# Kernel optimization log

Measured on AMD Instinct MI355X. Metric: run time of the kernel, lower is better.

The kernel has to match this reference:

```python
import jax, jax.numpy as jnp
import numpy as np

BATCH = 1048576
IN_DIM = 64   # input_dim = A.shape[1]
OUT_DIM = 16  # output_dim = A.shape[0]


def setup_inputs() -> dict:
    key = jax.random.key(0)
    k1, k2, k3 = jax.random.split(key, 3)
    y = jax.random.normal(k1, (BATCH, IN_DIM), dtype=jnp.float32)
    A = jax.random.normal(k2, (OUT_DIM, IN_DIM), dtype=jnp.float32)
    b = jax.random.normal(k3, (BATCH, OUT_DIM), dtype=jnp.float32)
    return {"y": y, "A": A, "b": b}


def _block_matrix(A):
    # KKT block matrix [[2I, A^T], [A, 0]], shape (n+m, n+m); shared across batch.
    m, n = A.shape
    Id2 = 2.0 * jnp.eye(n, dtype=A.dtype)
    top = jnp.concatenate([Id2, A.T], axis=1)          # (n, n+m)
    bot = jnp.concatenate([A, jnp.zeros((m, m), A.dtype)], axis=1)  # (m, n+m)
    return jnp.concatenate([top, bot], axis=0)


def reference(y, A, b):
    # Solve block_matrix @ sol_i = [2*y_i; b_i] for all samples i in one batched solve
    # (original torch code loops torch.linalg.solve over the batch with the SAME matrix).
    n = A.shape[1]
    M = _block_matrix(A)                               # (n+m, n+m)
    rhs = jnp.concatenate([2.0 * y, b], axis=1)        # (batch, n+m)
    sol = jnp.linalg.solve(M, rhs.T).T                 # factorize once, all RHS at once
    y_star = sol[:, :n]
    return y_star
```

## Files before the change

### kernel.cpp

```cpp
#include <hip/hip_runtime.h>

#define BATCH   1048576
#define IN_DIM  64
#define OUT_DIM 16

__global__ __launch_bounds__(256) void precompute_kernel(
    const float* __restrict__ A, float* __restrict__ ws)
{
    __shared__ float sA[16][64];
    __shared__ float M[16][32];
    __shared__ float fac[16];
    __shared__ int piv;

    const int tid = threadIdx.x;

    for (int i = tid; i < 1024; i += 256) sA[i >> 6][i & 63] = A[i];
    __syncthreads();

    {
        const int i = tid >> 4, j = tid & 15;
        float s = 0.f;
        #pragma unroll
        for (int k = 0; k < 64; ++k) s = fmaf(sA[i][k], sA[j][k], s);
        M[i][j] = s;
        M[i][16 + j] = (i == j) ? 1.f : 0.f;
    }
    __syncthreads();

    for (int p = 0; p < 16; ++p) {
        if (tid == 0) {
            int best = p;
            float bv = fabsf(M[p][p]);
            for (int r = p + 1; r < 16; ++r) {
                float v = fabsf(M[r][p]);
                if (v > bv) { bv = v; best = r; }
            }
            piv = best;
        }
        __syncthreads();
        if (tid < 32) {
            const int pr = piv;
            if (pr != p) { float t = M[p][tid]; M[p][tid] = M[pr][tid]; M[pr][tid] = t; }
        }
        __syncthreads();
        const float pv = M[p][p];
        __syncthreads();
        if (tid < 32) M[p][tid] *= (1.0f / pv);
        __syncthreads();
        if (tid < 16) fac[tid] = M[tid][p];
        __syncthreads();
        for (int e = tid; e < 512; e += 256) {
            const int r = e >> 5, c = e & 31;
            if (r != p) M[r][c] = fmaf(-fac[r], M[p][c], M[r][c]);
        }
        __syncthreads();
    }

    for (int e = tid; e < 1024; e += 256) {
        const int k = e >> 4, j = e & 15;
        ws[e] = sA[j][k];
    }
    for (int e = tid; e < 1024; e += 256) {
        const int k = e >> 4, i = e & 15;
        float s = 0.f;
        #pragma unroll
        for (int j = 0; j < 16; ++j) s = fmaf(M[i][16 + j], sA[j][k], s);
        ws[1024 + e] = s;
    }
}

__global__ __launch_bounds__(256)
__attribute__((amdgpu_waves_per_eu(4, 4)))
void apply_kernel(
    const float* __restrict__ y, const float* __restrict__ b,
    const float* __restrict__ ws, float* __restrict__ out)
{
    __shared__ float4 buf[4][64][8];

    const int tid  = threadIdx.x;
    const int wv   = tid >> 6;
    const int l    = tid & 63;
    const int srow = l >> 3;
    const int ssl  = l & 7;

    const float4* __restrict__ At4 = reinterpret_cast<const float4*>(ws);
    const float4* __restrict__ Ct4 = reinterpret_cast<const float4*>(ws + 1024);

    const size_t wbase = (size_t)blockIdx.x * 256 + (size_t)wv * 64;
    const float*  yb = y   + wbase * 64;
    float*        ob = out + wbase * 64;
    const float4* b4 = reinterpret_cast<const float4*>(b) + (wbase + l) * 4;

    float4 g0[8], g1[8];
    #pragma unroll
    for (int i = 0; i < 8; ++i)
        g0[i] = *reinterpret_cast<const float4*>(yb + (i * 8 + srow) * 64 + ssl * 4);
    #pragma unroll
    for (int i = 0; i < 8; ++i)
        g1[i] = *reinterpret_cast<const float4*>(yb + (i * 8 + srow) * 64 + 32 + ssl * 4);
    const float4 bv0 = b4[0], bv1 = b4[1], bv2 = b4[2], bv3 = b4[3];

    #pragma unroll
    for (int i = 0; i < 8; ++i) {
        const int row = i * 8 + srow;
        buf[wv][row][ssl ^ (row & 7)] = g0[i];
    }

    float t[16];
    t[ 0] = -bv0.x; t[ 1] = -bv0.y; t[ 2] = -bv0.z; t[ 3] = -bv0.w;
    t[ 4] = -bv1.x; t[ 5] = -bv1.y; t[ 6] = -bv1.z; t[ 7] = -bv1.w;
    t[ 8] = -bv2.x; t[ 9] = -bv2.y; t[10] = -bv2.z; t[11] = -bv2.w;
    t[12] = -bv3.x; t[13] = -bv3.y; t[14] = -bv3.z; t[15] = -bv3.w;

    float4 yr[8];
    #pragma unroll
    for (int q = 0; q < 8; ++q) {
        const float4 yv = buf[wv][l][q ^ (l & 7)];
        yr[q] = yv;
        #pragma unroll
        for (int dk = 0; dk < 4; ++dk) {
            const float yk = (dk == 0) ? yv.x : (dk == 1) ? yv.y :
                             (dk == 2) ? yv.z : yv.w;
            const int k = q * 4 + dk;
            #pragma unroll
            for (int jq = 0; jq < 4; ++jq) {
                const float4 a = At4[k * 4 + jq];
                t[4*jq+0] = fmaf(a.x, yk, t[4*jq+0]);
                t[4*jq+1] = fmaf(a.y, yk, t[4*jq+1]);
                t[4*jq+2] = fmaf(a.z, yk, t[4*jq+2]);
                t[4*jq+3] = fmaf(a.w, yk, t[4*jq+3]);
            }
        }
    }

    #pragma unroll
    for (int i = 0; i < 8; ++i) {
        const int row = i * 8 + srow;
        buf[wv][row][ssl ^ (row & 7)] = g1[i];
    }

    #pragma unroll
    for (int q = 0; q < 8; ++q) {
        const float4 yv = buf[wv][l][q ^ (l & 7)];
        #pragma unroll
        for (int dk = 0; dk < 4; ++dk) {
            const float yk = (dk == 0) ? yv.x : (dk == 1) ? yv.y :
                             (dk == 2) ? yv.z : yv.w;
            const int k = 32 + q * 4 + dk;
            #pragma unroll
            for (int jq = 0; jq < 4; ++jq) {
                const float4 a = At4[k * 4 + jq];
                t[4*jq+0] = fmaf(a.x, yk, t[4*jq+0]);
                t[4*jq+1] = fmaf(a.y, yk, t[4*jq+1]);
                t[4*jq+2] = fmaf(a.z, yk, t[4*jq+2]);
                t[4*jq+3] = fmaf(a.w, yk, t[4*jq+3]);
            }
        }
    }

    #pragma unroll
    for (int q = 0; q < 8; ++q) {
        const float4 yv = buf[wv][l][q ^ (l & 7)];
        float xv[4];
        #pragma unroll
        for (int dk = 0; dk < 4; ++dk) {
            const int k = 32 + q * 4 + dk;
            float x = (dk == 0) ? yv.x : (dk == 1) ? yv.y :
                      (dk == 2) ? yv.z : yv.w;
            #pragma unroll
            for (int iq = 0; iq < 4; ++iq) {
                const float4 c = Ct4[k * 4 + iq];
                x = fmaf(-c.x, t[4*iq+0], x);
                x = fmaf(-c.y, t[4*iq+1], x);
                x = fmaf(-c.z, t[4*iq+2], x);
                x = fmaf(-c.w, t[4*iq+3], x);
            }
            xv[dk] = x;
        }
        buf[wv][l][q ^ (l & 7)] = make_float4(xv[0], xv[1], xv[2], xv[3]);
    }
    #pragma unroll
    for (int i = 0; i < 8; ++i) {
        const int row = i * 8 + srow;
        *reinterpret_cast<float4*>(ob + row * 64 + 32 + ssl * 4) =
            buf[wv][row][ssl ^ (row & 7)];
    }

    #pragma unroll
    for (int q = 0; q < 8; ++q) {
        const float4 yv = yr[q];
        float xv[4];
        #pragma unroll
        for (int dk = 0; dk < 4; ++dk) {
            const int k = q * 4 + dk;
            float x = (dk == 0) ? yv.x : (dk == 1) ? yv.y :
                      (dk == 2) ? yv.z : yv.w;
            #pragma unroll
            for (int iq = 0; iq < 4; ++iq) {
                const float4 c = Ct4[k * 4 + iq];
                x = fmaf(-c.x, t[4*iq+0], x);
                x = fmaf(-c.y, t[4*iq+1], x);
                x = fmaf(-c.z, t[4*iq+2], x);
                x = fmaf(-c.w, t[4*iq+3], x);
            }
            xv[dk] = x;
        }
        buf[wv][l][q ^ (l & 7)] = make_float4(xv[0], xv[1], xv[2], xv[3]);
    }
    #pragma unroll
    for (int i = 0; i < 8; ++i) {
        const int row = i * 8 + srow;
        *reinterpret_cast<float4*>(ob + row * 64 + ssl * 4) =
            buf[wv][row][ssl ^ (row & 7)];
    }
}

extern "C" void kernel_launch(void* const* d_in, const int* in_sizes, int n_in,
                              void* d_out, int out_size, void* d_ws, size_t ws_size,
                              hipStream_t stream) {
    const float* y = (const float*)d_in[0];
    const float* A = (const float*)d_in[1];
    const float* b = (const float*)d_in[2];
    float* out = (float*)d_out;
    float* ws  = (float*)d_ws;

    precompute_kernel<<<1, 256, 0, stream>>>(A, ws);
    apply_kernel<<<BATCH / 256, 256, 0, stream>>>(y, b, ws, out);
}
```

Baseline: 165.0 us.

## Make apply kernel persistent-ish with two tiles per wave and software-prefetched loads

```diff
diff --git a/kernel.cpp b/kernel.cpp
--- a/kernel.cpp
+++ b/kernel.cpp
@@ -3,6 +3,8 @@
 #define BATCH   1048576
 #define IN_DIM  64
 #define OUT_DIM 16
+#define TPW     2
+#define NWTOT   8192
 
 __global__ __launch_bounds__(256) void precompute_kernel(
     const float* __restrict__ A, float* __restrict__ ws)
@@ -69,13 +71,11 @@
     }
 }
 
-__global__ __launch_bounds__(256)
-__attribute__((amdgpu_waves_per_eu(4, 4)))
-void apply_kernel(
+__global__ __launch_bounds__(128, 2) void apply_kernel(
     const float* __restrict__ y, const float* __restrict__ b,
     const float* __restrict__ ws, float* __restrict__ out)
 {
-    __shared__ float4 buf[4][64][8];
+    __shared__ float4 buf[2][64][16];
 
     const int tid  = threadIdx.x;
     const int wv   = tid >> 6;
@@ -86,132 +86,138 @@
     const float4* __restrict__ At4 = reinterpret_cast<const float4*>(ws);
     const float4* __restrict__ Ct4 = reinterpret_cast<const float4*>(ws + 1024);
 
-    const size_t wbase = (size_t)blockIdx.x * 256 + (size_t)wv * 64;
-    const float*  yb = y   + wbase * 64;
-    float*        ob = out + wbase * 64;
-    const float4* b4 = reinterpret_cast<const float4*>(b) + (wbase + l) * 4;
-
-    float4 g0[8], g1[8];
+    const size_t W = (size_t)blockIdx.x * 2 + wv;
+    size_t rowbase = W * 64;
+
+    float4 g[8];
+    {
+        const float* yb = y + rowbase * 64;
+        #pragma unroll
+        for (int i = 0; i < 8; ++i)
+            g[i] = *reinterpret_cast<const float4*>(yb + (i * 8 + srow) * 64 + ssl * 4);
+    }
+
     #pragma unroll
-    for (int i = 0; i < 8; ++i)
-        g0[i] = *reinterpret_cast<const float4*>(yb + (i * 8 + srow) * 64 + ssl * 4);
-    #pragma unroll
-    for (int i = 0; i < 8; ++i)
-        g1[i] = *reinterpret_cast<const float4*>(yb + (i * 8 + srow) * 64 + 32 + ssl * 4);
-    const float4 bv0 = b4[0], bv1 = b4[1], bv2 = b4[2], bv3 = b4[3];
-
-    #pragma unroll
-    for (int i = 0; i < 8; ++i) {
-        const int row = i * 8 + srow;
-        buf[wv][row][ssl ^ (row & 7)] = g0[i];
-    }
-
-    float t[16];
-    t[ 0] = -bv0.x; t[ 1] = -bv0.y; t[ 2] = -bv0.z; t[ 3] = -bv0.w;
-    t[ 4] = -bv1.x; t[ 5] = -bv1.y; t[ 6] = -bv1.z; t[ 7] = -bv1.w;
-    t[ 8] = -bv2.x; t[ 9] = -bv2.y; t[10] = -bv2.z; t[11] = -bv2.w;
-    t[12] = -bv3.x; t[13] = -bv3.y; t[14] = -bv3.z; t[15] = -bv3.w;
-
-    float4 yr[8];
-    #pragma unroll
-    for (int q = 0; q < 8; ++q) {
-        const float4 yv = buf[wv][l][q ^ (l & 7)];
-        yr[q] = yv;
-        #pragma unroll
-        for (int dk = 0; dk < 4; ++dk) {
-            const float yk = (dk == 0) ? yv.x : (dk == 1) ? yv.y :
-                             (dk == 2) ? yv.z : yv.w;
-            const int k = q * 4 + dk;
-            #pragma unroll
-            for (int jq = 0; jq < 4; ++jq) {
-                const float4 a = At4[k * 4 + jq];
-                t[4*jq+0] = fmaf(a.x, yk, t[4*jq+0]);
-                t[4*jq+1] = fmaf(a.y, yk, t[4*jq+1]);
-                t[4*jq+2] = fmaf(a.z, yk, t[4*jq+2]);
-                t[4*jq+3] = fmaf(a.w, yk, t[4*jq+3]);
-            }
-        }
-    }
-
-    #pragma unroll
-    for (int i = 0; i < 8; ++i) {
-        const int row = i * 8 + srow;
-        buf[wv][row][ssl ^ (row & 7)] = g1[i];
-    }
-
-    #pragma unroll
-    for (int q = 0; q < 8; ++q) {
-        const float4 yv = buf[wv][l][q ^ (l & 7)];
-        #pragma unroll
-        for (int dk = 0; dk < 4; ++dk) {
-            const float yk = (dk == 0) ? yv.x : (dk == 1) ? yv.y :
-                             (dk == 2) ? yv.z : yv.w;
-            const int k = 32 + q * 4 + dk;
-            #pragma unroll
-            for (int jq = 0; jq < 4; ++jq) {
-                const float4 a = At4[k * 4 + jq];
-                t[4*jq+0] = fmaf(a.x, yk, t[4*jq+0]);
-                t[4*jq+1] = fmaf(a.y, yk, t[4*jq+1]);
-                t[4*jq+2] = fmaf(a.z, yk, t[4*jq+2]);
-                t[4*jq+3] = fmaf(a.w, yk, t[4*jq+3]);
-            }
-        }
-    }
-
-    #pragma unroll
-    for (int q = 0; q < 8; ++q) {
-        const float4 yv = buf[wv][l][q ^ (l & 7)];
-        float xv[4];
-        #pragma unroll
-        for (int dk = 0; dk < 4; ++dk) {
-            const int k = 32 + q * 4 + dk;
-            float x = (dk == 0) ? yv.x : (dk == 1) ? yv.y :
-                      (dk == 2) ? yv.z : yv.w;
-            #pragma unroll
-            for (int iq = 0; iq < 4; ++iq) {
-                const float4 c = Ct4[k * 4 + iq];
-                x = fmaf(-c.x, t[4*iq+0], x);
-                x = fmaf(-c.y, t[4*iq+1], x);
-                x = fmaf(-c.z, t[4*iq+2], x);
-                x = fmaf(-c.w, t[4*iq+3], x);
-            }
-            xv[dk] = x;
-        }
-        buf[wv][l][q ^ (l & 7)] = make_float4(xv[0], xv[1], xv[2], xv[3]);
-    }
-    #pragma unroll
-    for (int i = 0; i < 8; ++i) {
-        const int row = i * 8 + srow;
-        *reinterpret_cast<float4*>(ob + row * 64 + 32 + ssl * 4) =
-            buf[wv][row][ssl ^ (row & 7)];
-    }
-
-    #pragma unroll
-    for (int q = 0; q < 8; ++q) {
-        const float4 yv = yr[q];
-        float xv[4];
-        #pragma unroll
-        for (int dk = 0; dk < 4; ++dk) {
-            const int k = q * 4 + dk;
-            float x = (dk == 0) ? yv.x : (dk == 1) ? yv.y :
-                      (dk == 2) ? yv.z : yv.w;
-            #pragma unroll
-            for (int iq = 0; iq < 4; ++iq) {
-                const float4 c = Ct4[k * 4 + iq];
-                x = fmaf(-c.x, t[4*iq+0], x);
-                x = fmaf(-c.y, t[4*iq+1], x);
-                x = fmaf(-c.z, t[4*iq+2], x);
-                x = fmaf(-c.w, t[4*iq+3], x);
-            }
-            xv[dk] = x;
-        }
-        buf[wv][l][q ^ (l & 7)] = make_float4(xv[0], xv[1], xv[2], xv[3]);
-    }
-    #pragma unroll
-    for (int i = 0; i < 8; ++i) {
-        const int row = i * 8 + srow;
-        *reinterpret_cast<float4*>(ob + row * 64 + ssl * 4) =
-            buf[wv][row][ssl ^ (row & 7)];
+    for (int s = 0; s < TPW; ++s) {
+        const float*  ybs = y   + rowbase * 64;
+        float*        obs = out + rowbase * 64;
+        const float4* b4  = reinterpret_cast<const float4*>(b) + (rowbase + l) * 4;
+
+        #pragma unroll
+        for (int i = 0; i < 8; ++i) {
+            const int row = i * 8 + srow;
+            buf[wv][row][ssl ^ (row & 7)] = g[i];
+        }
+        const float4 bv0 = b4[0], bv1 = b4[1], bv2 = b4[2], bv3 = b4[3];
+        #pragma unroll
+        for (int i = 0; i < 8; ++i)
+            g[i] = *reinterpret_cast<const float4*>(ybs + (i * 8 + srow) * 64 + 32 + ssl * 4);
+        __builtin_amdgcn_sched_barrier(0);
+
+        float t[16];
+        t[ 0] = -bv0.x; t[ 1] = -bv0.y; t[ 2] = -bv0.z; t[ 3] = -bv0.w;
+        t[ 4] = -bv1.x; t[ 5] = -bv1.y; t[ 6] = -bv1.z; t[ 7] = -bv1.w;
+        t[ 8] = -bv2.x; t[ 9] = -bv2.y; t[10] = -bv2.z; t[11] = -bv2.w;
+        t[12] = -bv3.x; t[13] = -bv3.y; t[14] = -bv3.z; t[15] = -bv3.w;
+
+        #pragma unroll
+        for (int q = 0; q < 8; ++q) {
+            const float4 yv = buf[wv][l][q ^ (l & 7)];
+            #pragma unroll
+            for (int dk = 0; dk < 4; ++dk) {
+                const float yk = (dk == 0) ? yv.x : (dk == 1) ? yv.y :
+                                 (dk == 2) ? yv.z : yv.w;
+                const int k = q * 4 + dk;
+                #pragma unroll
+                for (int jq = 0; jq < 4; ++jq) {
+                    const float4 a = At4[k * 4 + jq];
+                    t[4*jq+0] = fmaf(a.x, yk, t[4*jq+0]);
+                    t[4*jq+1] = fmaf(a.y, yk, t[4*jq+1]);
+                    t[4*jq+2] = fmaf(a.z, yk, t[4*jq+2]);
+                    t[4*jq+3] = fmaf(a.w, yk, t[4*jq+3]);
+                }
+            }
+        }
+
+        #pragma unroll
+        for (int i = 0; i < 8; ++i) {
+            const int row = i * 8 + srow;
+            buf[wv][row][8 + (ssl ^ (row & 7))] = g[i];
+        }
+        if (s + 1 < TPW) {
+            const float* yn = y + (rowbase + (size_t)NWTOT * 64) * 64;
+            #pragma unroll
+            for (int i = 0; i < 8; ++i)
+                g[i] = *reinterpret_cast<const float4*>(yn + (i * 8 + srow) * 64 + ssl * 4);
+        }
+        __builtin_amdgcn_sched_barrier(0);
+
+        #pragma unroll
+        for (int q = 0; q < 8; ++q) {
+            const float4 yv = buf[wv][l][8 + (q ^ (l & 7))];
+            #pragma unroll
+            for (int dk = 0; dk < 4; ++dk) {
+                const float yk = (dk == 0) ? yv.x : (dk == 1) ? yv.y :
+                                 (dk == 2) ? yv.z : yv.w;
+                const int k = 32 + q * 4 + dk;
+                #pragma unroll
+                for (int jq = 0; jq < 4; ++jq) {
+                    const float4 a = At4[k * 4 + jq];
+                    t[4*jq+0] = fmaf(a.x, yk, t[4*jq+0]);
+                    t[4*jq+1] = fmaf(a.y, yk, t[4*jq+1]);
+                    t[4*jq+2] = fmaf(a.z, yk, t[4*jq+2]);
+                    t[4*jq+3] = fmaf(a.w, yk, t[4*jq+3]);
+                }
+            }
+        }
+
+        #pragma unroll
+        for (int q = 0; q < 8; ++q) {
+            const float4 yv = buf[wv][l][q ^ (l & 7)];
+            float xv[4];
+            #pragma unroll
+            for (int dk = 0; dk < 4; ++dk) {
+                const int k = q * 4 + dk;
+                float x = (dk == 0) ? yv.x : (dk == 1) ? yv.y :
+                          (dk == 2) ? yv.z : yv.w;
+                #pragma unroll
+                for (int iq = 0; iq < 4; ++iq) {
+                    const float4 c = Ct4[k * 4 + iq];
+                    x = fmaf(-c.x, t[4*iq+0], x);
+                    x = fmaf(-c.y, t[4*iq+1], x);
+                    x = fmaf(-c.z, t[4*iq+2], x);
+                    x = fmaf(-c.w, t[4*iq+3], x);
+                }
+                xv[dk] = x;
+            }
+            *reinterpret_cast<float4*>(obs + l * 64 + q * 4) =
+                make_float4(xv[0], xv[1], xv[2], xv[3]);
+        }
+
+        #pragma unroll
+        for (int q = 0; q < 8; ++q) {
+            const float4 yv = buf[wv][l][8 + (q ^ (l & 7))];
+            float xv[4];
+            #pragma unroll
+            for (int dk = 0; dk < 4; ++dk) {
+                const int k = 32 + q * 4 + dk;
+                float x = (dk == 0) ? yv.x : (dk == 1) ? yv.y :
+                          (dk == 2) ? yv.z : yv.w;
+                #pragma unroll
+                for (int iq = 0; iq < 4; ++iq) {
+                    const float4 c = Ct4[k * 4 + iq];
+                    x = fmaf(-c.x, t[4*iq+0], x);
+                    x = fmaf(-c.y, t[4*iq+1], x);
+                    x = fmaf(-c.z, t[4*iq+2], x);
+                    x = fmaf(-c.w, t[4*iq+3], x);
+                }
+                xv[dk] = x;
+            }
+            *reinterpret_cast<float4*>(obs + l * 64 + 32 + q * 4) =
+                make_float4(xv[0], xv[1], xv[2], xv[3]);
+        }
+
+        rowbase += (size_t)NWTOT * 64;
     }
 }
 
@@ -225,5 +231,5 @@
     float* ws  = (float*)d_ws;
 
     precompute_kernel<<<1, 256, 0, stream>>>(A, ws);
-    apply_kernel<<<BATCH / 256, 256, 0, stream>>>(y, b, ws, out);
+    apply_kernel<<<NWTOT / 2, 128, 0, stream>>>(y, b, ws, out);
 }
```

Result: slower. 562.4 us (+240.8%).
